# Optimization experiments

Measured on AMD Instinct MI355X. Metric: run time of the kernel, lower is better.

## Reference

```python
import jax, jax.numpy as jnp
import numpy as np

EPS_NORM = 1e-12   # torch F.normalize eps
EPS_TRIP = 1e-6    # torch pairwise_distance eps
MARGIN = 1.0

def _l2_normalize(x, axis=1):
    n = jnp.linalg.norm(x, axis=axis, keepdims=True)
    return x / jnp.maximum(n, EPS_NORM)

def setup_inputs() -> dict:
    key = jax.random.key(0)
    k1, k2 = jax.random.split(key)
    bs, m, d = 32768, 2048, 256
    query = jax.random.normal(k1, (bs, d), dtype=jnp.float32)
    memory = jax.random.normal(k2, (m, d), dtype=jnp.float32)
    return {"query": query, "memory": memory}

def reference(query, memory):
    m, d = memory.shape
    q = _l2_normalize(query, axis=1)                      # [bs, d]
    score = jnp.matmul(q, memory.T)                       # [bs, m]
    sfx_score_query = jax.nn.softmax(score, axis=0)       # softmax over batch
    sfx_score_memory = jax.nn.softmax(score, axis=1)      # softmax over slots

    # --- update (note: original passes sfx_score_query for BOTH score args) ---
    max_idx = jnp.argmax(sfx_score_query, axis=1)         # [bs] topk(k=1) over dim=1
    colmax = jnp.max(sfx_score_query, axis=0)             # [m]
    sel = jnp.take_along_axis(sfx_score_query, max_idx[:, None], axis=1)[:, 0]  # score[j, max_idx[j]]
    w = sel / colmax[max_idx]                              # [bs]
    # vectorized form of the per-slot gather/weighted-sum loop (segment-sum)
    query_update = jax.ops.segment_sum(w[:, None] * q, max_idx, num_segments=m)  # [m, d]
    updated_memory = jax.lax.stop_gradient(_l2_normalize(query_update + memory, axis=1))

    # --- read (uses ORIGINAL memory in the train path) ---
    concat_memory = jnp.matmul(jax.lax.stop_gradient(sfx_score_memory), memory)  # [bs, d]
    update_query = jnp.concatenate([q, concat_memory], axis=1)                   # [bs, 2d]

    # --- losses (computed from sfx_score_memory as intended) ---
    top2_vals, top2_idx = jax.lax.top_k(sfx_score_memory, 2)
    pos = jax.lax.stop_gradient(memory[top2_idx[:, 0]])   # [bs, d]
    neg = jax.lax.stop_gradient(memory[top2_idx[:, 1]])   # [bs, d]
    gathering_loss = jnp.mean((q - pos) ** 2)
    d_pos = jnp.linalg.norm(q - pos + EPS_TRIP, axis=1)
    d_neg = jnp.linalg.norm(q - neg + EPS_TRIP, axis=1)
    spreading_loss = jnp.mean(jnp.maximum(d_pos - d_neg + MARGIN, 0.0))

    return (update_query, updated_memory, sfx_score_query, sfx_score_memory,
            gathering_loss, spreading_loss)
```

## Files before the change

### kernel.cpp

```cpp
#include <hip/hip_runtime.h>
#include <hip/hip_bf16.h>
#include <cstddef>
#include <cstdint>

#define BS 32768
#define MSLOT 2048
#define D 256
#define NCHUNK 256

typedef _Float16 f16;
typedef _Float16 f16x8 __attribute__((ext_vector_type(8)));
typedef float f32x4 __attribute__((ext_vector_type(4)));

__device__ __forceinline__ void lds_cp16(void* dst, const void* src) {
    __builtin_amdgcn_global_load_lds(
        (const __attribute__((address_space(1))) void*)src,
        (__attribute__((address_space(3))) void*)dst, 16, 0, 0);
}

__device__ __forceinline__ void top2_merge(float& a0, int& ai0, float& a1, int& ai1,
                                           float b0, int bi0, float b1, int bi1)
{
    bool bt = (b0 > a0) || (b0 == a0 && bi0 < ai0);
    float n0, n1; int ni0, ni1;
    if (bt) {
        n0 = b0; ni0 = bi0;
        bool s2 = (b1 > a0) || (b1 == a0 && bi1 < ai0);
        n1 = s2 ? b1 : a0; ni1 = s2 ? bi1 : ai0;
    } else {
        n0 = a0; ni0 = ai0;
        bool s2 = (b0 > a1) || (b0 == a1 && bi0 < ai1);
        n1 = s2 ? b0 : a1; ni1 = s2 ? bi0 : ai1;
    }
    a0 = n0; ai0 = ni0; a1 = n1; ai1 = ni1;
}

__global__ __launch_bounds__(256) void k_prepq(const float* __restrict__ query,
                                               float* __restrict__ out0,
                                               f16* __restrict__ qh, f16* __restrict__ ql)
{
    __shared__ float sbuf[4];
    const int i = blockIdx.x, t = threadIdx.x;
    float v = query[(size_t)i * D + t];
    float ss = v * v;
#pragma unroll
    for (int off = 32; off; off >>= 1) ss += __shfl_xor(ss, off, 64);
    if ((t & 63) == 0) sbuf[t >> 6] = ss;
    __syncthreads();
    float tot = (sbuf[0] + sbuf[1]) + (sbuf[2] + sbuf[3]);
    float n = fmaxf(sqrtf(tot), 1e-12f);
    float qv = v / n;
    out0[(size_t)i * (2 * D) + t] = qv;
    float qs = qv * 256.0f;
    f16 h = (f16)qs;
    f16 lo = (f16)(qs - (float)h);
    qh[(size_t)i * D + t] = h;
    ql[(size_t)i * D + t] = lo;
}

__global__ __launch_bounds__(256) void k_prepm(const float* __restrict__ memory,
                                               f16* __restrict__ mh, f16* __restrict__ ml,
                                               f16* __restrict__ memT,
                                               float* __restrict__ qupd)
{
    const int j = blockIdx.x, t = threadIdx.x;
    float m = memory[(size_t)j * D + t];
    f16 h = (f16)m;
    f16 lo = (f16)(m - (float)h);
    mh[(size_t)j * D + t] = h;
    ml[(size_t)j * D + t] = lo;
    memT[(size_t)t * MSLOT + j] = h;
    qupd[(size_t)j * D + t] = 0.0f;
}

__global__ __launch_bounds__(256) void k_score(const f16* __restrict__ qh, const f16* __restrict__ ql,
                                               const f16* __restrict__ mh, const f16* __restrict__ ml,
                                               float* __restrict__ out2,
                                               float* __restrict__ colpart)
{
    __shared__ __align__(16) f16 Ah[2][4096], Al[2][4096], Bh[2][4096], Bl[2][4096];
    __shared__ float sepM[4][4][16], sepS[4][4][16];
    const int t = threadIdx.x;
    const int l = t & 63, w = t >> 6;
    const int wr = w >> 1, wc = w & 1;
    const int lk = l >> 4, lm = l & 15;
    const int i0 = blockIdx.y * 128, j0 = blockIdx.x * 128;

    f32x4 acc[4][4] = {};

#define STAGE_SCORE(buf, k0)                                                     \
    {                                                                            \
        _Pragma("unroll")                                                        \
        for (int c = 0; c < 2; ++c) {                                            \
            int s = c * 256 + t;                                                 \
            int r = s >> 2, cc = s & 3;                                          \
            int scc = cc ^ ((r >> 1) & 3);                                       \
            size_t aoff = (size_t)(i0 + r) * D + (k0) + scc * 8;                 \
            size_t boff = (size_t)(j0 + r) * D + (k0) + scc * 8;                 \
            lds_cp16(&Ah[buf][s * 8], qh + aoff);                                \
            lds_cp16(&Al[buf][s * 8], ql + aoff);                                \
            lds_cp16(&Bh[buf][s * 8], mh + boff);                                \
            lds_cp16(&Bl[buf][s * 8], ml + boff);                                \
        }                                                                        \
    }

    STAGE_SCORE(0, 0);
    __syncthreads();

    for (int ks = 0; ks < 8; ++ks) {
        const int cur = ks & 1;
        if (ks < 7) STAGE_SCORE(cur ^ 1, (ks + 1) * 32);

        f16x8 a_h[4], a_l[4], b_h[4], b_l[4];
#pragma unroll
        for (int m = 0; m < 4; ++m) {
            int r = wr * 64 + m * 16 + lm;
            int off = r * 64 + ((lk ^ ((r >> 1) & 3)) << 4);
            a_h[m] = *(const f16x8*)((const char*)Ah[cur] + off);
            a_l[m] = *(const f16x8*)((const char*)Al[cur] + off);
        }
#pragma unroll
        for (int n = 0; n < 4; ++n) {
            int r = wc * 64 + n * 16 + lm;
            int off = r * 64 + ((lk ^ ((r >> 1) & 3)) << 4);
            b_h[n] = *(const f16x8*)((const char*)Bh[cur] + off);
            b_l[n] = *(const f16x8*)((const char*)Bl[cur] + off);
        }
#pragma unroll
        for (int m = 0; m < 4; ++m)
#pragma unroll
            for (int n = 0; n < 4; ++n) {
                acc[m][n] = __builtin_amdgcn_mfma_f32_16x16x32_f16(a_h[m], b_h[n], acc[m][n], 0, 0, 0);
                acc[m][n] = __builtin_amdgcn_mfma_f32_16x16x32_f16(a_h[m], b_l[n], acc[m][n], 0, 0, 0);
                acc[m][n] = __builtin_amdgcn_mfma_f32_16x16x32_f16(a_l[m], b_h[n], acc[m][n], 0, 0, 0);
            }
        __syncthreads();
    }
#undef STAGE_SCORE

    const float sc = 1.0f / 256.0f;
#pragma unroll
    for (int m = 0; m < 4; ++m)
#pragma unroll
        for (int n = 0; n < 4; ++n)
            acc[m][n] *= sc;

#pragma unroll
    for (int m = 0; m < 4; ++m) {
        int row = i0 + wr * 64 + m * 16 + lk * 4;
#pragma unroll
        for (int n = 0; n < 4; ++n) {
            int col = j0 + wc * 64 + n * 16 + lm;
#pragma unroll
            for (int r = 0; r < 4; ++r)
                out2[(size_t)(row + r) * MSLOT + col] = acc[m][n][r];
        }
    }

    float cm[4], cs[4];
#pragma unroll
    for (int n = 0; n < 4; ++n) {
        float mx = -INFINITY;
#pragma unroll
        for (int m = 0; m < 4; ++m)
#pragma unroll
            for (int r = 0; r < 4; ++r) mx = fmaxf(mx, acc[m][n][r]);
        float sm = 0.0f;
#pragma unroll
        for (int m = 0; m < 4; ++m)
#pragma unroll
            for (int r = 0; r < 4; ++r) sm += __expf(acc[m][n][r] - mx);
#pragma unroll
        for (int off = 16; off <= 32; off <<= 1) {
            float om = __shfl_xor(mx, off, 64);
            float os = __shfl_xor(sm, off, 64);
            float nm = fmaxf(mx, om);
            sm = sm * __expf(mx - nm) + os * __expf(om - nm);
            mx = nm;
        }
        cm[n] = mx; cs[n] = sm;
    }
    if (l < 16) {
#pragma unroll
        for (int n = 0; n < 4; ++n) { sepM[w][n][l] = cm[n]; sepS[w][n][l] = cs[n]; }
    }
    __syncthreads();
    if (w < 2 && l < 16) {
#pragma unroll
        for (int n = 0; n < 4; ++n) {
            float m1 = sepM[w][n][l], s1 = sepS[w][n][l];
            float m2 = sepM[w + 2][n][l], s2 = sepS[w + 2][n][l];
            float nm = fmaxf(m1, m2);
            float ns = s1 * __expf(m1 - nm) + s2 * __expf(m2 - nm);
            int col = j0 + w * 64 + n * 16 + l;
            size_t o = ((size_t)blockIdx.y * MSLOT + col) * 2;
            colpart[o + 0] = nm;
            colpart[o + 1] = ns;
        }
    }
}

__global__ __launch_bounds__(256) void k_colmerge(const float* __restrict__ colpart,
                                                  float* __restrict__ colM,
                                                  float* __restrict__ colSinv,
                                                  float* __restrict__ colC)
{
    const int col = blockIdx.x * 256 + threadIdx.x;
    float m = -INFINITY, s = 0.0f;
    for (int c = 0; c < NCHUNK; ++c) {
        size_t o = ((size_t)c * MSLOT + col) * 2;
        float pm = colpart[o + 0], ps = colpart[o + 1];
        float nm = fmaxf(m, pm);
        s = s * __expf(m - nm) + ps * __expf(pm - nm);
        m = nm;
    }
    colM[col] = m;
    colSinv[col] = 1.0f / s;
    colC[col] = m + __logf(s);
}

__global__ __launch_bounds__(256) void k_rowtrans(float* __restrict__ sq,
                                                  float* __restrict__ sm,
                                                  f16* __restrict__ pf16,
                                                  const float* __restrict__ colM,
                                                  const float* __restrict__ colSinv,
                                                  const float* __restrict__ colC,
                                                  const float* __restrict__ out0,
                                                  const float* __restrict__ memory,
                                                  int* __restrict__ jstarA, float* __restrict__ wA,
                                                  float* __restrict__ gpart, float* __restrict__ spart)
{
    __shared__ float swm[4], sws[4];
    __shared__ float st0v[4], st1v[4]; __shared__ int st0i[4], st1i[4];
    __shared__ float sav[4], sar[4];  __shared__ int sai[4];
    __shared__ float sg[4], sdp[4], sdn[4];

    const int i = blockIdx.x, t = threadIdx.x;
    const int l = t & 63, w = t >> 6;
    const int jb = t * 8;
    float* row = sq + (size_t)i * MSLOT;

    float v[8];
    {
        float4 va = *(const float4*)(row + jb);
        float4 vb = *(const float4*)(row + jb + 4);
        v[0] = va.x; v[1] = va.y; v[2] = va.z; v[3] = va.w;
        v[4] = vb.x; v[5] = vb.y; v[6] = vb.z; v[7] = vb.w;
    }
    float cCv[8], cMv[8], cSv[8];
    {
        float4 a = *(const float4*)(colC + jb);
        float4 b = *(const float4*)(colC + jb + 4);
        cCv[0] = a.x; cCv[1] = a.y; cCv[2] = a.z; cCv[3] = a.w;
        cCv[4] = b.x; cCv[5] = b.y; cCv[6] = b.z; cCv[7] = b.w;
        a = *(const float4*)(colM + jb); b = *(const float4*)(colM + jb + 4);
        cMv[0] = a.x; cMv[1] = a.y; cMv[2] = a.z; cMv[3] = a.w;
        cMv[4] = b.x; cMv[5] = b.y; cMv[6] = b.z; cMv[7] = b.w;
        a = *(const float4*)(colSinv + jb); b = *(const float4*)(colSinv + jb + 4);
        cSv[0] = a.x; cSv[1] = a.y; cSv[2] = a.z; cSv[3] = a.w;
        cSv[4] = b.x; cSv[5] = b.y; cSv[6] = b.z; cSv[7] = b.w;
    }

    float lmx = v[0];
#pragma unroll
    for (int k = 1; k < 8; ++k) lmx = fmaxf(lmx, v[k]);
#pragma unroll
    for (int off = 32; off; off >>= 1) lmx = fmaxf(lmx, __shfl_xor(lmx, off, 64));
    if (l == 0) swm[w] = lmx;
    __syncthreads();
    const float rm = fmaxf(fmaxf(swm[0], swm[1]), fmaxf(swm[2], swm[3]));

    float ls = 0.0f;
#pragma unroll
    for (int k = 0; k < 8; ++k) ls += __expf(v[k] - rm);

    float v0 = -INFINITY, v1 = -INFINITY; int i0 = 0x7fffffff, i1 = 0x7fffffff;
#pragma unroll
    for (int k = 0; k < 8; ++k) {
        int idx = jb + k; float cv = v[k];
        if (cv > v0)      { v1 = v0; i1 = i0; v0 = cv; i0 = idx; }
        else if (cv > v1) { v1 = cv; i1 = idx; }
    }

    float av = -INFINITY, araw = 0.0f; int ai = 0x7fffffff;
#pragma unroll
    for (int k = 0; k < 8; ++k) {
        int idx = jb + k;
        float x = v[k] - cCv[k];
        if (x > av) { av = x; ai = idx; araw = v[k]; }
    }

#pragma unroll
    for (int off = 32; off; off >>= 1) ls += __shfl_xor(ls, off, 64);
#pragma unroll
    for (int off = 1; off < 64; off <<= 1) {
        float b0 = __shfl_xor(v0, off, 64), b1 = __shfl_xor(v1, off, 64);
        int  bi0 = __shfl_xor(i0, off, 64), bi1 = __shfl_xor(i1, off, 64);
        top2_merge(v0, i0, v1, i1, b0, bi0, b1, bi1);
    }
#pragma unroll
    for (int off = 1; off < 64; off <<= 1) {
        float ov = __shfl_xor(av, off, 64), oraw = __shfl_xor(araw, off, 64);
        int   oi = __shfl_xor(ai, off, 64);
        if (ov > av || (ov == av && oi < ai)) { av = ov; ai = oi; araw = oraw; }
    }
    if (l == 0) {
        sws[w] = ls;
        st0v[w] = v0; st0i[w] = i0; st1v[w] = v1; st1i[w] = i1;
        sav[w] = av; sai[w] = ai; sar[w] = araw;
    }
    __syncthreads();

    const float rs = (sws[0] + sws[1]) + (sws[2] + sws[3]);
    const float rsinv = 1.0f / rs;

    float T0 = -INFINITY, T1 = -INFINITY; int I0 = 0x7fffffff, I1 = 0x7fffffff;
#pragma unroll
    for (int ww = 0; ww < 4; ++ww)
        top2_merge(T0, I0, T1, I1, st0v[ww], st0i[ww], st1v[ww], st1i[ww]);

    float AV = -INFINITY, AR = 0.0f; int AI = 0x7fffffff;
#pragma unroll
    for (int ww = 0; ww < 4; ++ww) {
        if (sav[ww] > AV || (sav[ww] == AV && sai[ww] < AI)) { AV = sav[ww]; AI = sai[ww]; AR = sar[ww]; }
    }

    float qv = out0[(size_t)i * (2 * D) + t];
    float pv = memory[(size_t)I0 * D + t];
    float nv = memory[(size_t)I1 * D + t];
    float dq = qv - pv;
    float g  = dq * dq;
    float dp = dq + 1e-6f;          dp *= dp;
    float dn = (qv - nv) + 1e-6f;   dn *= dn;
#pragma unroll
    for (int off = 32; off; off >>= 1) {
        g  += __shfl_xor(g, off, 64);
        dp += __shfl_xor(dp, off, 64);
        dn += __shfl_xor(dn, off, 64);
    }
    if (l == 0) { sg[w] = g; sdp[w] = dp; sdn[w] = dn; }
    __syncthreads();
    if (t == 0) {
        float gs  = (sg[0] + sg[1]) + (sg[2] + sg[3]);
        float dps = (sdp[0] + sdp[1]) + (sdp[2] + sdp[3]);
        float dns = (sdn[0] + sdn[1]) + (sdn[2] + sdn[3]);
        gpart[i] = gs;
        spart[i] = fmaxf(sqrtf(dps) - sqrtf(dns) + 1.0f, 0.0f);
        jstarA[i] = AI;
        wA[i] = __expf(AR - colM[AI]);
    }

    float oq[8], om[8];
#pragma unroll
    for (int k = 0; k < 8; ++k) {
        oq[k] = __expf(v[k] - cMv[k]) * cSv[k];
        om[k] = __expf(v[k] - rm) * rsinv;
    }
    float4 q0 = {oq[0], oq[1], oq[2], oq[3]}, q1 = {oq[4], oq[5], oq[6], oq[7]};
    float4 m0 = {om[0], om[1], om[2], om[3]}, m1 = {om[4], om[5], om[6], om[7]};
    *(float4*)(row + jb) = q0;
    *(float4*)(row + jb + 4) = q1;
    *(float4*)(sm + (size_t)i * MSLOT + jb) = m0;
    *(float4*)(sm + (size_t)i * MSLOT + jb + 4) = m1;
    f16x8 h;
#pragma unroll
    for (int k = 0; k < 8; ++k) h[k] = (f16)om[k];
    *(f16x8*)(pf16 + (size_t)i * MSLOT + jb) = h;
}

__global__ __launch_bounds__(256) void k_scatter(const f16* __restrict__ qh,
                                                 const f16* __restrict__ ql,
                                                 const int* __restrict__ jstarA,
                                                 const float* __restrict__ wA,
                                                 float* __restrict__ qupd)
{
    const int i = blockIdx.x, t = threadIdx.x;
    const int j = jstarA[i];
    const float wv = wA[i] * (1.0f / 256.0f);
    float qv = (float)qh[(size_t)i * D + t] + (float)ql[(size_t)i * D + t];
    unsafeAtomicAdd(&qupd[(size_t)j * D + t], wv * qv);
}

__global__ __launch_bounds__(256) void k_updmem(const float* __restrict__ qupd,
                                                const float* __restrict__ memory,
                                                float* __restrict__ out1)
{
    __shared__ float sbuf[4];
    const int j = blockIdx.x, t = threadIdx.x;
    float v = qupd[(size_t)j * D + t] + memory[(size_t)j * D + t];
    float ss = v * v;
#pragma unroll
    for (int off = 32; off; off >>= 1) ss += __shfl_xor(ss, off, 64);
    if ((t & 63) == 0) sbuf[t >> 6] = ss;
    __syncthreads();
    float tot = (sbuf[0] + sbuf[1]) + (sbuf[2] + sbuf[3]);
    float n = fmaxf(sqrtf(tot), 1e-12f);
    out1[(size_t)j * D + t] = v / n;
}

__global__ __launch_bounds__(256) void k_concat(const f16* __restrict__ P,
                                                const f16* __restrict__ memT,
                                                float* __restrict__ out0)
{
    __shared__ __align__(16) f16 As[2][4096];
    __shared__ __align__(16) f16 Bs[2][8192];
    const int t = threadIdx.x;
    const int l = t & 63, w = t >> 6;
    const int lk = l >> 4, lm = l & 15;
    const int i0 = blockIdx.x * 128;

#define STAGE_CC(buf, k0)                                                        \
    {                                                                            \
        _Pragma("unroll")                                                        \
        for (int c = 0; c < 2; ++c) {                                            \
            int s = c * 256 + t;                                                 \
            int r = s >> 2, cc = s & 3;                                          \
            int scc = cc ^ ((r >> 1) & 3);                                       \
            lds_cp16(&As[buf][s * 8], P + (size_t)(i0 + r) * MSLOT + (k0) + scc * 8); \
        }                                                                        \
        _Pragma("unroll")                                                        \
        for (int c = 0; c < 4; ++c) {                                            \
            int s = c * 256 + t;                                                 \
            int n = s >> 2, cc = s & 3;                                          \
            int scc = cc ^ ((n >> 1) & 3);                                       \
            lds_cp16(&Bs[buf][s * 8], memT + (size_t)n * MSLOT + (k0) + scc * 8); \
        }                                                                        \
    }

    f32x4 acc[2][16] = {};
    STAGE_CC(0, 0);
    __syncthreads();

    for (int ks = 0; ks < 64; ++ks) {
        const int cur = ks & 1;
        if (ks < 63) STAGE_CC(cur ^ 1, (ks + 1) * 32);

        f16x8 af[2];
#pragma unroll
        for (int m = 0; m < 2; ++m) {
            int r = w * 32 + m * 16 + lm;
            int off = r * 64 + ((lk ^ ((r >> 1) & 3)) << 4);
            af[m] = *(const f16x8*)((const char*)As[cur] + off);
        }
#pragma unroll
        for (int hh = 0; hh < 2; ++hh) {
            f16x8 bf[8];
#pragma unroll
            for (int n = 0; n < 8; ++n) {
                int r = (hh * 8 + n) * 16 + lm;
                int off = r * 64 + ((lk ^ ((r >> 1) & 3)) << 4);
                bf[n] = *(const f16x8*)((const char*)Bs[cur] + off);
            }
#pragma unroll
            for (int m = 0; m < 2; ++m)
#pragma unroll
                for (int n = 0; n < 8; ++n)
                    acc[m][hh * 8 + n] = __builtin_amdgcn_mfma_f32_16x16x32_f16(af[m], bf[n], acc[m][hh * 8 + n], 0, 0, 0);
        }
        __syncthreads();
    }
#undef STAGE_CC

#pragma unroll
    for (int m = 0; m < 2; ++m) {
        int row = i0 + w * 32 + m * 16 + lk * 4;
#pragma unroll
        for (int n = 0; n < 16; ++n) {
            int col = n * 16 + lm;
#pragma unroll
            for (int r = 0; r < 4; ++r)
                out0[(size_t)(row + r) * (2 * D) + D + col] = acc[m][n][r];
        }
    }
}

__global__ __launch_bounds__(256) void k_losses(const float* __restrict__ gpart,
                                                const float* __restrict__ spart,
                                                float* __restrict__ out45)
{
    __shared__ float sf[256];
    const int t = threadIdx.x;
    float g = 0.f, s = 0.f;
    for (int i = t; i < BS; i += 256) { g += gpart[i]; s += spart[i]; }
    sf[t] = g; __syncthreads();
    for (int off = 128; off; off >>= 1) { if (t < off) sf[t] += sf[t + off]; __syncthreads(); }
    float gt = sf[0]; __syncthreads();
    sf[t] = s; __syncthreads();
    for (int off = 128; off; off >>= 1) { if (t < off) sf[t] += sf[t + off]; __syncthreads(); }
    float st = sf[0];
    if (t == 0) {
        out45[0] = gt / (float)((size_t)BS * D);
        out45[1] = st / (float)BS;
    }
}

extern "C" void kernel_launch(void* const* d_in, const int* in_sizes, int n_in,
                              void* d_out, int out_size, void* d_ws, size_t ws_size,
                              hipStream_t stream)
{
    const float* query  = (const float*)d_in[0];
    const float* memory = (const float*)d_in[1];

    float* out  = (float*)d_out;
    float* out0 = out;
    float* out1 = out0 + (size_t)BS * 2 * D;
    float* out2 = out1 + (size_t)MSLOT * D;
    float* out3 = out2 + (size_t)BS * MSLOT;
    float* out45 = out3 + (size_t)BS * MSLOT;

    f16* qh   = (f16*)d_ws;
    f16* ql   = qh + (size_t)BS * D;
    f16* mh   = ql + (size_t)BS * D;
    f16* ml   = mh + (size_t)MSLOT * D;
    f16* memT = ml + (size_t)MSLOT * D;
    f16* pf16 = memT + (size_t)D * MSLOT;
    float* colpart = (float*)(pf16 + (size_t)BS * MSLOT);
    float* colM    = colpart + (size_t)NCHUNK * MSLOT * 2;
    float* colSinv = colM + MSLOT;
    float* colC    = colSinv + MSLOT;
    float* wA      = colC + MSLOT;
    int*   jstarA  = (int*)(wA + BS);
    float* gpart   = (float*)(jstarA + BS);
    float* spart   = gpart + BS;
    float* qupd    = spart + BS;

    k_prepq<<<BS, 256, 0, stream>>>(query, out0, qh, ql);
    k_prepm<<<MSLOT, 256, 0, stream>>>(memory, mh, ml, memT, qupd);

    k_score<<<dim3(MSLOT / 128, BS / 128), 256, 0, stream>>>(qh, ql, mh, ml, out2, colpart);

    k_colmerge<<<MSLOT / 256, 256, 0, stream>>>(colpart, colM, colSinv, colC);

    k_rowtrans<<<BS, 256, 0, stream>>>(out2, out3, pf16, colM, colSinv, colC, out0, memory,
                                       jstarA, wA, gpart, spart);

    k_scatter<<<BS, 256, 0, stream>>>(qh, ql, jstarA, wA, qupd);
    k_updmem<<<MSLOT, 256, 0, stream>>>(qupd, memory, out1);

    k_concat<<<BS / 128, 256, 0, stream>>>(pf16, memT, out0);

    k_losses<<<1, 256, 0, stream>>>(gpart, spart, out45);
}
```

Baseline: 640.9 us.

## Rework score and concat GEMMs with larger tiles and concatenated hi/lo operands

The hi/lo split f16 operands are packed into one contiguous 512-wide row per query and memory slot. The score GEMM then becomes a single K=768 pass that covers hi*hi, hi*lo and lo*hi, instead of issuing three MFMAs per step. Score tiles grow to 256x256 with 512 threads, a swizzled XCD-aware block mapping, 64-wide K stages with explicit vmcnt waits, raw barriers and setprio. The concat GEMM gets the same pipeline with 512 threads and 64-wide K. NCHUNK is halved to match the new row-tile count. Larger tiles raise register and LDS pressure and reduce the number of blocks in flight.

```diff
diff --git a/kernel.cpp b/kernel.cpp
--- a/kernel.cpp
+++ b/kernel.cpp
@@ -6,11 +6,19 @@
 #define BS 32768
 #define MSLOT 2048
 #define D 256
-#define NCHUNK 256
+#define NCHUNK 128
 
 typedef _Float16 f16;
 typedef _Float16 f16x8 __attribute__((ext_vector_type(8)));
 typedef float f32x4 __attribute__((ext_vector_type(4)));
+
+#define WAITV(n) asm volatile("s_waitcnt vmcnt(" #n ")" ::: "memory")
+
+__device__ __forceinline__ void barrier_raw() {
+    asm volatile("" ::: "memory");
+    __builtin_amdgcn_s_barrier();
+    asm volatile("" ::: "memory");
+}
 
 __device__ __forceinline__ void lds_cp16(void* dst, const void* src) {
     __builtin_amdgcn_global_load_lds(
@@ -37,7 +45,7 @@
 
 __global__ __launch_bounds__(256) void k_prepq(const float* __restrict__ query,
                                                float* __restrict__ out0,
-                                               f16* __restrict__ qh, f16* __restrict__ ql)
+                                               f16* __restrict__ qcat)
 {
     __shared__ float sbuf[4];
     const int i = blockIdx.x, t = threadIdx.x;
@@ -54,12 +62,12 @@
     float qs = qv * 256.0f;
     f16 h = (f16)qs;
     f16 lo = (f16)(qs - (float)h);
-    qh[(size_t)i * D + t] = h;
-    ql[(size_t)i * D + t] = lo;
+    qcat[(size_t)i * 512 + t] = h;
+    qcat[(size_t)i * 512 + 256 + t] = lo;
 }
 
 __global__ __launch_bounds__(256) void k_prepm(const float* __restrict__ memory,
-                                               f16* __restrict__ mh, f16* __restrict__ ml,
+                                               f16* __restrict__ mcat,
                                                f16* __restrict__ memT,
                                                float* __restrict__ qupd)
 {
@@ -67,109 +75,117 @@
     float m = memory[(size_t)j * D + t];
     f16 h = (f16)m;
     f16 lo = (f16)(m - (float)h);
-    mh[(size_t)j * D + t] = h;
-    ml[(size_t)j * D + t] = lo;
+    mcat[(size_t)j * 512 + t] = h;
+    mcat[(size_t)j * 512 + 256 + t] = lo;
     memT[(size_t)t * MSLOT + j] = h;
     qupd[(size_t)j * D + t] = 0.0f;
 }
 
-__global__ __launch_bounds__(256) void k_score(const f16* __restrict__ qh, const f16* __restrict__ ql,
-                                               const f16* __restrict__ mh, const f16* __restrict__ ml,
-                                               float* __restrict__ out2,
-                                               float* __restrict__ colpart)
-{
-    __shared__ __align__(16) f16 Ah[2][4096], Al[2][4096], Bh[2][4096], Bl[2][4096];
-    __shared__ float sepM[4][4][16], sepS[4][4][16];
-    const int t = threadIdx.x;
-    const int l = t & 63, w = t >> 6;
-    const int wr = w >> 1, wc = w & 1;
-    const int lk = l >> 4, lm = l & 15;
-    const int i0 = blockIdx.y * 128, j0 = blockIdx.x * 128;
-
-    f32x4 acc[4][4] = {};
-
-#define STAGE_SCORE(buf, k0)                                                     \
-    {                                                                            \
-        _Pragma("unroll")                                                        \
-        for (int c = 0; c < 2; ++c) {                                            \
-            int s = c * 256 + t;                                                 \
-            int r = s >> 2, cc = s & 3;                                          \
-            int scc = cc ^ ((r >> 1) & 3);                                       \
-            size_t aoff = (size_t)(i0 + r) * D + (k0) + scc * 8;                 \
-            size_t boff = (size_t)(j0 + r) * D + (k0) + scc * 8;                 \
-            lds_cp16(&Ah[buf][s * 8], qh + aoff);                                \
-            lds_cp16(&Al[buf][s * 8], ql + aoff);                                \
-            lds_cp16(&Bh[buf][s * 8], mh + boff);                                \
-            lds_cp16(&Bl[buf][s * 8], ml + boff);                                \
-        }                                                                        \
-    }
-
-    STAGE_SCORE(0, 0);
-    __syncthreads();
-
-    for (int ks = 0; ks < 8; ++ks) {
-        const int cur = ks & 1;
-        if (ks < 7) STAGE_SCORE(cur ^ 1, (ks + 1) * 32);
-
-        f16x8 a_h[4], a_l[4], b_h[4], b_l[4];
-#pragma unroll
-        for (int m = 0; m < 4; ++m) {
-            int r = wr * 64 + m * 16 + lm;
-            int off = r * 64 + ((lk ^ ((r >> 1) & 3)) << 4);
-            a_h[m] = *(const f16x8*)((const char*)Ah[cur] + off);
-            a_l[m] = *(const f16x8*)((const char*)Al[cur] + off);
+__global__ __launch_bounds__(512, 2) void k_score(const f16* __restrict__ qcat,
+                                                  const f16* __restrict__ mcat,
+                                                  float* __restrict__ out2,
+                                                  float* __restrict__ colpart)
+{
+    __shared__ __align__(16) f16 As[2][256 * 64];
+    __shared__ __align__(16) f16 Bs[2][256 * 64];
+    __shared__ float sepM[8][4][16], sepS[8][4][16];
+
+    const int tid = threadIdx.x;
+    const int l = tid & 63, w = tid >> 6;
+    const int wr = w >> 2, wc = w & 3;
+    const int lk = (l >> 4) & 3, lm = l & 15;
+    const int sr = tid >> 3, sch = tid & 7;
+
+    const int hflat = blockIdx.y * 8 + blockIdx.x;
+    const int xcd = hflat & 7, kk8 = hflat >> 3;
+    const int by = xcd * 16 + (kk8 >> 3);
+    const int bx = kk8 & 7;
+    const int i0 = by * 256, j0 = bx * 256;
+
+#define STAGE(buf, t) do {                                                          \
+    int k0_ = (t) * 64;                                                             \
+    int ao_ = ((t) < 8 ? 0 : 256) + (k0_ & 255);                                    \
+    int bo_ = ((((t) >= 4) && ((t) < 8)) ? 256 : 0) + (k0_ & 255);                  \
+    _Pragma("unroll")                                                               \
+    for (int c = 0; c < 4; ++c) {                                                   \
+        int r_ = c * 64 + sr;                                                       \
+        int g_ = sch ^ ((r_ >> 1) & 7);                                             \
+        lds_cp16(&As[buf][(c * 512 + tid) * 8],                                     \
+                 qcat + (size_t)(i0 + r_) * 512 + ao_ + g_ * 8);                    \
+        lds_cp16(&Bs[buf][(c * 512 + tid) * 8],                                     \
+                 mcat + (size_t)(j0 + r_) * 512 + bo_ + g_ * 8);                    \
+    }                                                                               \
+} while (0)
+
+    f32x4 acc[8][4] = {};
+
+    STAGE(0, 0);
+    STAGE(1, 1);
+
+    for (int t = 0; t < 12; ++t) {
+        const int cur = t & 1;
+        if (t < 11) { WAITV(8); } else { WAITV(0); }
+        barrier_raw();
+        const f16* Ab = As[cur];
+        const f16* Bb = Bs[cur];
+        __builtin_amdgcn_s_setprio(1);
+#pragma unroll
+        for (int kk = 0; kk < 2; ++kk) {
+            f16x8 bf[4];
+#pragma unroll
+            for (int ni = 0; ni < 4; ++ni) {
+                int r = wc * 64 + ni * 16 + lm;
+                int slot = (kk * 4 + lk) ^ (lm >> 1);
+                bf[ni] = *(const f16x8*)(Bb + r * 64 + slot * 8);
+            }
+#pragma unroll
+            for (int mi = 0; mi < 8; ++mi) {
+                int r = wr * 128 + mi * 16 + lm;
+                int slot = (kk * 4 + lk) ^ (lm >> 1);
+                f16x8 af = *(const f16x8*)(Ab + r * 64 + slot * 8);
+#pragma unroll
+                for (int ni = 0; ni < 4; ++ni)
+                    acc[mi][ni] = __builtin_amdgcn_mfma_f32_16x16x32_f16(af, bf[ni], acc[mi][ni], 0, 0, 0);
+            }
         }
-#pragma unroll
-        for (int n = 0; n < 4; ++n) {
-            int r = wc * 64 + n * 16 + lm;
-            int off = r * 64 + ((lk ^ ((r >> 1) & 3)) << 4);
-            b_h[n] = *(const f16x8*)((const char*)Bh[cur] + off);
-            b_l[n] = *(const f16x8*)((const char*)Bl[cur] + off);
+        __builtin_amdgcn_s_setprio(0);
+        barrier_raw();
+        if (t < 10) STAGE(cur, t + 2);
+    }
+#undef STAGE
+
+    const float sc = 1.0f / 256.0f;
+#pragma unroll
+    for (int mi = 0; mi < 8; ++mi)
+#pragma unroll
+        for (int ni = 0; ni < 4; ++ni)
+            acc[mi][ni] *= sc;
+
+#pragma unroll
+    for (int mi = 0; mi < 8; ++mi) {
+        int row = i0 + wr * 128 + mi * 16 + lk * 4;
+#pragma unroll
+        for (int ni = 0; ni < 4; ++ni) {
+            int col = j0 + wc * 64 + ni * 16 + lm;
+#pragma unroll
+            for (int r = 0; r < 4; ++r)
+                out2[(size_t)(row + r) * MSLOT + col] = acc[mi][ni][r];
         }
-#pragma unroll
-        for (int m = 0; m < 4; ++m)
-#pragma unroll
-            for (int n = 0; n < 4; ++n) {
-                acc[m][n] = __builtin_amdgcn_mfma_f32_16x16x32_f16(a_h[m], b_h[n], acc[m][n], 0, 0, 0);
-                acc[m][n] = __builtin_amdgcn_mfma_f32_16x16x32_f16(a_h[m], b_l[n], acc[m][n], 0, 0, 0);
-                acc[m][n] = __builtin_amdgcn_mfma_f32_16x16x32_f16(a_l[m], b_h[n], acc[m][n], 0, 0, 0);
-            }
-        __syncthreads();
-    }
-#undef STAGE_SCORE
-
-    const float sc = 1.0f / 256.0f;
-#pragma unroll
-    for (int m = 0; m < 4; ++m)
-#pragma unroll
-        for (int n = 0; n < 4; ++n)
-            acc[m][n] *= sc;
-
-#pragma unroll
-    for (int m = 0; m < 4; ++m) {
-        int row = i0 + wr * 64 + m * 16 + lk * 4;
-#pragma unroll
-        for (int n = 0; n < 4; ++n) {
-            int col = j0 + wc * 64 + n * 16 + lm;
-#pragma unroll
-            for (int r = 0; r < 4; ++r)
-                out2[(size_t)(row + r) * MSLOT + col] = acc[m][n][r];
-        }
     }
 
     float cm[4], cs[4];
 #pragma unroll
-    for (int n = 0; n < 4; ++n) {
+    for (int ni = 0; ni < 4; ++ni) {
         float mx = -INFINITY;
 #pragma unroll
-        for (int m = 0; m < 4; ++m)
-#pragma unroll
-            for (int r = 0; r < 4; ++r) mx = fmaxf(mx, acc[m][n][r]);
+        for (int mi = 0; mi < 8; ++mi)
+#pragma unroll
+            for (int r = 0; r < 4; ++r) mx = fmaxf(mx, acc[mi][ni][r]);
         float sm = 0.0f;
 #pragma unroll
-        for (int m = 0; m < 4; ++m)
-#pragma unroll
-            for (int r = 0; r < 4; ++r) sm += __expf(acc[m][n][r] - mx);
+        for (int mi = 0; mi < 8; ++mi)
+#pragma unroll
+            for (int r = 0; r < 4; ++r) sm += __expf(acc[mi][ni][r] - mx);
 #pragma unroll
         for (int off = 16; off <= 32; off <<= 1) {
             float om = __shfl_xor(mx, off, 64);
@@ -178,22 +194,22 @@
             sm = sm * __expf(mx - nm) + os * __expf(om - nm);
             mx = nm;
         }
-        cm[n] = mx; cs[n] = sm;
+        cm[ni] = mx; cs[ni] = sm;
     }
     if (l < 16) {
 #pragma unroll
-        for (int n = 0; n < 4; ++n) { sepM[w][n][l] = cm[n]; sepS[w][n][l] = cs[n]; }
+        for (int ni = 0; ni < 4; ++ni) { sepM[w][ni][l] = cm[ni]; sepS[w][ni][l] = cs[ni]; }
     }
     __syncthreads();
-    if (w < 2 && l < 16) {
-#pragma unroll
-        for (int n = 0; n < 4; ++n) {
-            float m1 = sepM[w][n][l], s1 = sepS[w][n][l];
-            float m2 = sepM[w + 2][n][l], s2 = sepS[w + 2][n][l];
+    if (w < 4 && l < 16) {
+#pragma unroll
+        for (int ni = 0; ni < 4; ++ni) {
+            float m1 = sepM[w][ni][l], s1 = sepS[w][ni][l];
+            float m2 = sepM[w + 4][ni][l], s2 = sepS[w + 4][ni][l];
             float nm = fmaxf(m1, m2);
             float ns = s1 * __expf(m1 - nm) + s2 * __expf(m2 - nm);
-            int col = j0 + w * 64 + n * 16 + l;
-            size_t o = ((size_t)blockIdx.y * MSLOT + col) * 2;
+            int col = j0 + w * 64 + ni * 16 + l;
+            size_t o = ((size_t)by * MSLOT + col) * 2;
             colpart[o + 0] = nm;
             colpart[o + 1] = ns;
         }
@@ -368,8 +384,7 @@
     *(f16x8*)(pf16 + (size_t)i * MSLOT + jb) = h;
 }
 
-__global__ __launch_bounds__(256) void k_scatter(const f16* __restrict__ qh,
-                                                 const f16* __restrict__ ql,
+__global__ __launch_bounds__(256) void k_scatter(const f16* __restrict__ qcat,
                                                  const int* __restrict__ jstarA,
                                                  const float* __restrict__ wA,
                                                  float* __restrict__ qupd)
@@ -377,7 +392,7 @@
     const int i = blockIdx.x, t = threadIdx.x;
     const int j = jstarA[i];
     const float wv = wA[i] * (1.0f / 256.0f);
-    float qv = (float)qh[(size_t)i * D + t] + (float)ql[(size_t)i * D + t];
+    float qv = (float)qcat[(size_t)i * 512 + t] + (float)qcat[(size_t)i * 512 + 256 + t];
     unsafeAtomicAdd(&qupd[(size_t)j * D + t], wv * qv);
 }
 
@@ -398,78 +413,83 @@
     out1[(size_t)j * D + t] = v / n;
 }
 
-__global__ __launch_bounds__(256) void k_concat(const f16* __restrict__ P,
-                                                const f16* __restrict__ memT,
-                                                float* __restrict__ out0)
-{
-    __shared__ __align__(16) f16 As[2][4096];
-    __shared__ __align__(16) f16 Bs[2][8192];
-    const int t = threadIdx.x;
-    const int l = t & 63, w = t >> 6;
-    const int lk = l >> 4, lm = l & 15;
+__global__ __launch_bounds__(512, 2) void k_concat(const f16* __restrict__ P,
+                                                   const f16* __restrict__ memT,
+                                                   float* __restrict__ out0)
+{
+    __shared__ __align__(16) f16 As[2][128 * 64];
+    __shared__ __align__(16) f16 Bs[2][256 * 64];
+    const int tid = threadIdx.x;
+    const int l = tid & 63, w = tid >> 6;
+    const int wr = w >> 2, wc = w & 3;
+    const int lk = (l >> 4) & 3, lm = l & 15;
+    const int sr = tid >> 3, sch = tid & 7;
     const int i0 = blockIdx.x * 128;
 
-#define STAGE_CC(buf, k0)                                                        \
-    {                                                                            \
-        _Pragma("unroll")                                                        \
-        for (int c = 0; c < 2; ++c) {                                            \
-            int s = c * 256 + t;                                                 \
-            int r = s >> 2, cc = s & 3;                                          \
-            int scc = cc ^ ((r >> 1) & 3);                                       \
-            lds_cp16(&As[buf][s * 8], P + (size_t)(i0 + r) * MSLOT + (k0) + scc * 8); \
-        }                                                                        \
-        _Pragma("unroll")                                                        \
-        for (int c = 0; c < 4; ++c) {                                            \
-            int s = c * 256 + t;                                                 \
-            int n = s >> 2, cc = s & 3;                                          \
-            int scc = cc ^ ((n >> 1) & 3);                                       \
-            lds_cp16(&Bs[buf][s * 8], memT + (size_t)n * MSLOT + (k0) + scc * 8); \
-        }                                                                        \
-    }
-
-    f32x4 acc[2][16] = {};
+#define STAGE_CC(buf, t) do {                                                       \
+    int k0_ = (t) * 64;                                                             \
+    _Pragma("unroll")                                                               \
+    for (int c = 0; c < 2; ++c) {                                                   \
+        int r_ = c * 64 + sr;                                                       \
+        int g_ = sch ^ ((r_ >> 1) & 7);                                             \
+        lds_cp16(&As[buf][(c * 512 + tid) * 8],                                     \
+                 P + (size_t)(i0 + r_) * MSLOT + k0_ + g_ * 8);                     \
+    }                                                                               \
+    _Pragma("unroll")                                                               \
+    for (int c = 0; c < 4; ++c) {                                                   \
+        int r_ = c * 64 + sr;                                                       \
+        int g_ = sch ^ ((r_ >> 1) & 7);                                             \
+        lds_cp16(&Bs[buf][(c * 512 + tid) * 8],                                     \
+                 memT + (size_t)r_ * MSLOT + k0_ + g_ * 8);                         \
+    }                                                                               \
+} while (0)
+
+    f32x4 acc[4][4] = {};
+
     STAGE_CC(0, 0);
-    __syncthreads();
-
-    for (int ks = 0; ks < 64; ++ks) {
-        const int cur = ks & 1;
-        if (ks < 63) STAGE_CC(cur ^ 1, (ks + 1) * 32);
-
-        f16x8 af[2];
-#pragma unroll
-        for (int m = 0; m < 2; ++m) {
-            int r = w * 32 + m * 16 + lm;
-            int off = r * 64 + ((lk ^ ((r >> 1) & 3)) << 4);
-            af[m] = *(const f16x8*)((const char*)As[cur] + off);
+    STAGE_CC(1, 1);
+
+    for (int t = 0; t < 32; ++t) {
+        const int cur = t & 1;
+        if (t < 31) { WAITV(6); } else { WAITV(0); }
+        barrier_raw();
+        const f16* Ab = As[cur];
+        const f16* Bb = Bs[cur];
+        __builtin_amdgcn_s_setprio(1);
+#pragma unroll
+        for (int kk = 0; kk < 2; ++kk) {
+            f16x8 bf[4];
+#pragma unroll
+            for (int ni = 0; ni < 4; ++ni) {
+                int r = wc * 64 + ni * 16 + lm;
+                int slot = (kk * 4 + lk) ^ (lm >> 1);
+                bf[ni] = *(const f16x8*)(Bb + r * 64 + slot * 8);
+            }
+#pragma unroll
+            for (int mi = 0; mi < 4; ++mi) {
+                int r = wr * 64 + mi * 16 + lm;
+                int slot = (kk * 4 + lk) ^ (lm >> 1);
+                f16x8 af = *(const f16x8*)(Ab + r * 64 + slot * 8);
+#pragma unroll
+                for (int ni = 0; ni < 4; ++ni)
+                    acc[mi][ni] = __builtin_amdgcn_mfma_f32_16x16x32_f16(af, bf[ni], acc[mi][ni], 0, 0, 0);
+            }
         }
-#pragma unroll
-        for (int hh = 0; hh < 2; ++hh) {
-            f16x8 bf[8];
-#pragma unroll
-            for (int n = 0; n < 8; ++n) {
-                int r = (hh * 8 + n) * 16 + lm;
-                int off = r * 64 + ((lk ^ ((r >> 1) & 3)) << 4);
-                bf[n] = *(const f16x8*)((const char*)Bs[cur] + off);
-            }
-#pragma unroll
-            for (int m = 0; m < 2; ++m)
-#pragma unroll
-                for (int n = 0; n < 8; ++n)
-                    acc[m][hh * 8 + n] = __builtin_amdgcn_mfma_f32_16x16x32_f16(af[m], bf[n], acc[m][hh * 8 + n], 0, 0, 0);
-        }
-        __syncthreads();
+        __builtin_amdgcn_s_setprio(0);
+        barrier_raw();
+        if (t < 30) STAGE_CC(cur, t + 2);
     }
 #undef STAGE_CC
 
 #pragma unroll
-    for (int m = 0; m < 2; ++m) {
-        int row = i0 + w * 32 + m * 16 + lk * 4;
-#pragma unroll
-        for (int n = 0; n < 16; ++n) {
-            int col = n * 16 + lm;
+    for (int mi = 0; mi < 4; ++mi) {
+        int row = i0 + wr * 64 + mi * 16 + lk * 4;
+#pragma unroll
+        for (int ni = 0; ni < 4; ++ni) {
+            int col = wc * 64 + ni * 16 + lm;
 #pragma unroll
             for (int r = 0; r < 4; ++r)
-                out0[(size_t)(row + r) * (2 * D) + D + col] = acc[m][n][r];
+                out0[(size_t)(row + r) * (2 * D) + D + col] = acc[mi][ni][r];
         }
     }
 }
@@ -508,11 +528,9 @@
     float* out3 = out2 + (size_t)BS * MSLOT;
     float* out45 = out3 + (size_t)BS * MSLOT;
 
-    f16* qh   = (f16*)d_ws;
-    f16* ql   = qh + (size_t)BS * D;
-    f16* mh   = ql + (size_t)BS * D;
-    f16* ml   = mh + (size_t)MSLOT * D;
-    f16* memT = ml + (size_t)MSLOT * D;
+    f16* qcat = (f16*)d_ws;
+    f16* mcat = qcat + (size_t)BS * 512;
+    f16* memT = mcat + (size_t)MSLOT * 512;
     f16* pf16 = memT + (size_t)D * MSLOT;
     float* colpart = (float*)(pf16 + (size_t)BS * MSLOT);
     float* colM    = colpart + (size_t)NCHUNK * MSLOT * 2;
@@ -524,20 +542,20 @@
     float* spart   = gpart + BS;
     float* qupd    = spart + BS;
 
-    k_prepq<<<BS, 256, 0, stream>>>(query, out0, qh, ql);
-    k_prepm<<<MSLOT, 256, 0, stream>>>(memory, mh, ml, memT, qupd);
-
-    k_score<<<dim3(MSLOT / 128, BS / 128), 256, 0, stream>>>(qh, ql, mh, ml, out2, colpart);
+    k_prepq<<<BS, 256, 0, stream>>>(query, out0, qcat);
+    k_prepm<<<MSLOT, 256, 0, stream>>>(memory, mcat, memT, qupd);
+
+    k_score<<<dim3(MSLOT / 256, BS / 256), 512, 0, stream>>>(qcat, mcat, out2, colpart);
 
     k_colmerge<<<MSLOT / 256, 256, 0, stream>>>(colpart, colM, colSinv, colC);
 
     k_rowtrans<<<BS, 256, 0, stream>>>(out2, out3, pf16, colM, colSinv, colC, out0, memory,
                                        jstarA, wA, gpart, spart);
 
-    k_scatter<<<BS, 256, 0, stream>>>(qh, ql, jstarA, wA, qupd);
+    k_scatter<<<BS, 256, 0, stream>>>(qcat, jstarA, wA, qupd);
     k_updmem<<<MSLOT, 256, 0, stream>>>(qupd, memory, out1);
 
-    k_concat<<<BS / 128, 256, 0, stream>>>(pf16, memT, out0);
+    k_concat<<<BS / 128, 512, 0, stream>>>(pf16, memT, out0);
 
     k_losses<<<1, 256, 0, stream>>>(gpart, spart, out45);
 }
```

Measured after the change: 578.2 us. 1.11x faster.
